# Performance work log

Hardware: AMD Instinct MI355X
Metric: run time of the kernel (lower is better)

Reference implementation:

```python
import jax, jax.numpy as jnp
import numpy as np

VOCAB = 100
EMB = 256
HID = 256
B = 8
S = 2048


def setup_inputs() -> dict:
    key = jax.random.key(0)
    ks = jax.random.split(key, 12)
    s_e = 1.0 / np.sqrt(EMB)
    s_h = 1.0 / np.sqrt(HID)
    return {
        "x": jax.random.randint(ks[0], (B, S), 0, VOCAB),
        "embedding": jax.random.normal(ks[1], (VOCAB, EMB), jnp.float32),
        "w_ih": jax.random.uniform(ks[2], (3 * HID, EMB), jnp.float32, -s_e, s_e),
        "w_hh": jax.random.uniform(ks[3], (3 * HID, HID), jnp.float32, -s_h, s_h),
        "b_ih": jax.random.uniform(ks[4], (3 * HID,), jnp.float32, -s_h, s_h),
        "b_hh": jax.random.uniform(ks[5], (3 * HID,), jnp.float32, -s_h, s_h),
        "attn_w": jax.random.uniform(ks[6], (HID, HID), jnp.float32, -s_h, s_h),
        "attn_b": jax.random.uniform(ks[7], (HID,), jnp.float32, -s_h, s_h),
        "comb_w": jax.random.uniform(ks[8], (HID, 2 * HID), jnp.float32, -s_h, s_h),
        "comb_b": jax.random.uniform(ks[9], (HID,), jnp.float32, -s_h, s_h),
        "fc_w": jax.random.uniform(ks[10], (VOCAB, HID), jnp.float32, -s_h, s_h),
        "fc_b": jax.random.uniform(ks[11], (VOCAB,), jnp.float32, -s_h, s_h),
    }


def _gru(emb, w_ih, w_hh, b_ih, b_hh):
    # emb: [B, S, E]; PyTorch GRU gate order: r, z, n
    xg = jnp.einsum('bse,ge->bsg', emb, w_ih) + b_ih  # [B, S, 3H]
    h0 = jnp.zeros((emb.shape[0], HID), emb.dtype)

    def step(h, xg_t):
        hg = h @ w_hh.T + b_hh
        xr, xz, xn = jnp.split(xg_t, 3, axis=-1)
        hr, hz, hn = jnp.split(hg, 3, axis=-1)
        r = jax.nn.sigmoid(xr + hr)
        z = jax.nn.sigmoid(xz + hz)
        n = jnp.tanh(xn + r * hn)
        h_new = (1.0 - z) * n + z * h
        return h_new, h_new

    h_last, hs = jax.lax.scan(step, h0, jnp.swapaxes(xg, 0, 1))
    return jnp.swapaxes(hs, 0, 1), h_last  # [B,S,H], [B,H]


def reference(x, embedding, w_ih, w_hh, b_ih, b_hh, attn_w, attn_b, comb_w, comb_b, fc_w, fc_b):
    emb = embedding[x]  # [B, S, E]
    all_h, h_last = _gru(emb, w_ih, w_hh, b_ih, b_hh)
    keys = jnp.einsum('bsh,kh->bsk', all_h, attn_w) + attn_b  # [B,S,H]
    scores = jnp.einsum('bqh,bkh->bqk', all_h, keys)  # [B,S,S]
    seq = all_h.shape[1]
    causal = jnp.tril(jnp.ones((seq, seq), bool))
    scores = jnp.where(causal[None], scores, -jnp.inf)
    attn = jax.nn.softmax(scores, axis=-1)
    context = jnp.einsum('bqk,bkh->bqh', attn, all_h)  # [B,S,H]
    combined = jnp.concatenate([all_h, context], axis=-1)
    combined = jnp.tanh(jnp.einsum('bsd,hd->bsh', combined, comb_w) + comb_b)
    output = jnp.einsum('bsh,vh->bsv', combined, fc_w) + fc_b
    return output, h_last[None]  # hidden: [num_layers=1, B, H]
```

## Files before the change

### kernel.cpp

```cpp
#include <hip/hip_runtime.h>

#define SEQ  2048
#define NB   8
#define HD   256
#define G3   768
#define NV   100
#define KVB  32

typedef float f32x4 __attribute__((ext_vector_type(4)));
typedef int   i32x4 __attribute__((ext_vector_type(4)));
typedef short s16x8 __attribute__((ext_vector_type(8)));
typedef unsigned short u16x4 __attribute__((ext_vector_type(4)));

#define INV26 1.490116119384765625e-8f

__device__ __forceinline__ float rcp_fast(float x) {
  return __builtin_amdgcn_rcpf(x);
}
__device__ __forceinline__ float sigm(float x) {
  x = fminf(fmaxf(x, -30.f), 30.f);
  return rcp_fast(1.f + __expf(-x));
}
__device__ __forceinline__ float tanh_fast(float x) {
  x = fminf(fmaxf(x, -15.f), 15.f);
  float e = __expf(2.f * x);
  return (e - 1.f) * rcp_fast(e + 1.f);
}
__device__ __forceinline__ void cvt_hilo(float f, unsigned short& h, unsigned short& l) {
  unsigned u = __float_as_uint(f);
  h = (unsigned short)(u >> 16);
  float r = f - __uint_as_float(u & 0xffff0000u);
  l = (unsigned short)(__float_as_uint(r) >> 16);
}

__global__ __launch_bounds__(256) void build_table(
    const float* __restrict__ emb, const float* __restrict__ w_ih,
    const float* __restrict__ b_ih, float* __restrict__ table) {
  __shared__ float eL[256];
  __shared__ float wL[256][37];
  int v = blockIdx.x, tid = threadIdx.x;
  eL[tid] = emb[v * HD + tid];
  for (int gt = 0; gt < 3; ++gt) {
    float acc = b_ih[gt * 256 + tid];
    for (int e0 = 0; e0 < HD; e0 += 32) {
      __syncthreads();
      #pragma unroll
      for (int i = 0; i < 32; ++i) {
        int idx = tid + i * 256;
        int r = idx >> 5, c = idx & 31;
        wL[r][c] = w_ih[(size_t)(gt * 256 + r) * HD + e0 + c];
      }
      __syncthreads();
      #pragma unroll
      for (int c = 0; c < 32; ++c) acc += eL[e0 + c] * wL[tid][c];
    }
    table[((size_t)v * 256 + tid) * 4 + gt] = acc;
  }
}

__global__ void __launch_bounds__(512) gru_scan(
    const int* __restrict__ x, const float* __restrict__ w_hh,
    const float* __restrict__ b_hh, const float* __restrict__ table,
    float* __restrict__ all_h, float* __restrict__ h_last) {
  __shared__ __align__(16) signed char hpk[2][2 * 272];
  __shared__ int xs[SEQ];
  const int b = blockIdx.x;
  int tid = threadIdx.x;
  int lane = tid & 63, wv = tid >> 6;
  int ncol = lane & 15, quad = lane >> 4;
  int usel = quad & 1;
  int j = wv * 32 + usel * 16 + ncol;

  for (int i = tid; i < SEQ; i += 512) xs[i] = x[b * SEQ + i];
  for (int i = tid; i < 2 * 272; i += 512)
    hpk[0][i] = (i >= 272) ? (signed char)-128 : 0;

  i32x4 bw[2][3][4];
  float Cn2[2][3];
  #pragma unroll
  for (int u = 0; u < 2; ++u) {
    #pragma unroll
    for (int t3 = 0; t3 < 3; ++t3) {
      int row = t3 * 256 + wv * 32 + u * 16 + ncol;
      int sw = 0;
      #pragma unroll
      for (int c = 0; c < 4; ++c) {
        const float* p = w_hh + (size_t)row * HD + c * 64 + quad * 16;
        unsigned pw[4] = {0u, 0u, 0u, 0u};
        #pragma unroll
        for (int e = 0; e < 16; ++e) {
          int q = __float2int_rn(p[e] * 2048.f);
          q = max(-127, min(127, q));
          sw += q;
          pw[e >> 2] |= ((unsigned)(q & 255)) << ((e & 3) * 8);
        }
        bw[u][t3][c] = (i32x4){(int)pw[0], (int)pw[1], (int)pw[2], (int)pw[3]};
      }
      sw += __shfl_xor(sw, 16);
      sw += __shfl_xor(sw, 32);
      Cn2[u][t3] = b_hh[row] + 128.f * (float)sw * INV26;
    }
  }
  float Csel[3];
  #pragma unroll
  for (int t3 = 0; t3 < 3; ++t3) Csel[t3] = usel ? Cn2[1][t3] : Cn2[0][t3];

  float hreg = 0.f;
  __syncthreads();
  float xr, xz, xn;
  {
    int v = xs[0];
    f32x4 xg = *(const f32x4*)&table[((size_t)v * 256 + j) * 4];
    xr = xg[0]; xz = xg[1]; xn = xg[2];
  }
  int a_base = (ncol & 1) * 272 + quad * 16;

  for (int t = 0; t < SEQ; ++t) {
    const signed char* cb = hpk[t & 1];
    i32x4 a[4];
    #pragma unroll
    for (int c = 0; c < 4; ++c)
      a[c] = *(const i32x4*)&cb[a_base + c * 64];
    float hg[3];
    #pragma unroll
    for (int t3 = 0; t3 < 3; ++t3) {
      i32x4 A0 = {0, 0, 0, 0}, A1 = {0, 0, 0, 0};
      #pragma unroll
      for (int c = 0; c < 4; ++c) {
        A0 = __builtin_amdgcn_mfma_i32_16x16x64_i8(a[c], bw[0][t3][c], A0, 0, 0, 0);
        A1 = __builtin_amdgcn_mfma_i32_16x16x64_i8(a[c], bw[1][t3][c], A1, 0, 0, 0);
      }
      int d0 = usel ? A1[0] : A0[0];
      int d1 = usel ? A1[1] : A0[1];
      hg[t3] = ((float)d0 * 256.f + (float)d1) * INV26 + Csel[t3];
    }
    float r = sigm(xr + hg[0]);
    float z = sigm(xz + hg[1]);
    float n = tanh_fast(xn + r * hg[2]);
    float h = (1.f - z) * n + z * hreg;
    hreg = h;
    int q = min(__float2int_rn(h * 32768.f), 32767);
    int lou = q & 255;
    int hi8 = (q - lou) >> 8;
    signed char* nx = hpk[(t + 1) & 1];
    if (quad < 2) {
      nx[j] = (signed char)hi8;
      nx[272 + j] = (signed char)(lou - 128);
      all_h[((size_t)b * SEQ + t) * HD + j] = h;
    }
    int v = xs[(t + 1 < SEQ) ? t + 1 : t];
    f32x4 xg = *(const f32x4*)&table[((size_t)v * 256 + j) * 4];
    xr = xg[0]; xz = xg[1]; xn = xg[2];
    __syncthreads();
  }
  if (quad < 2) h_last[b * HD + j] = hreg;
}

template<int ACT>
__global__ __launch_bounds__(256) void gemm_bias(
    const float* __restrict__ A, int lda,
    const float* __restrict__ W, const float* __restrict__ bias,
    float* __restrict__ C, int ldc, int N, int K) {
  __shared__ float As[128][36];
  __shared__ float Ws[64][36];
  int tid = threadIdx.x;
  int m0 = blockIdx.y * 128, n0 = blockIdx.x * 64;
  int ml = tid & 31, g = tid >> 5;
  float acc[4][8];
  #pragma unroll
  for (int i = 0; i < 4; ++i)
    #pragma unroll
    for (int jj = 0; jj < 8; ++jj) acc[i][jj] = 0.f;
  for (int k0 = 0; k0 < K; k0 += 32) {
    __syncthreads();
    #pragma unroll
    for (int i = 0; i < 4; ++i) {
      int idx = tid + i * 256;
      int r = idx >> 3, c4 = (idx & 7) * 4;
      *(f32x4*)&As[r][c4] = *(const f32x4*)&A[(size_t)(m0 + r) * lda + k0 + c4];
    }
    #pragma unroll
    for (int i = 0; i < 2; ++i) {
      int idx = tid + i * 256;
      int r = idx >> 3, c4 = (idx & 7) * 4;
      f32x4 wv = {0.f, 0.f, 0.f, 0.f};
      if (n0 + r < N) wv = *(const f32x4*)&W[(size_t)(n0 + r) * K + k0 + c4];
      *(f32x4*)&Ws[r][c4] = wv;
    }
    __syncthreads();
    #pragma unroll
    for (int k4 = 0; k4 < 32; k4 += 4) {
      f32x4 av[4], wv8[8];
      #pragma unroll
      for (int i = 0; i < 4; ++i) av[i] = *(const f32x4*)&As[ml + i * 32][k4];
      #pragma unroll
      for (int jj = 0; jj < 8; ++jj) wv8[jj] = *(const f32x4*)&Ws[g * 8 + jj][k4];
      #pragma unroll
      for (int kk = 0; kk < 4; ++kk)
        #pragma unroll
        for (int i = 0; i < 4; ++i)
          #pragma unroll
          for (int jj = 0; jj < 8; ++jj)
            acc[i][jj] += av[i][kk] * wv8[jj][kk];
    }
  }
  #pragma unroll
  for (int i = 0; i < 4; ++i) {
    int m = m0 + ml + i * 32;
    #pragma unroll
    for (int jj = 0; jj < 8; ++jj) {
      int n = n0 + g * 8 + jj;
      if (n < N) {
        float val = acc[i][jj] + bias[n];
        if (ACT) val = tanh_fast(val);
        C[(size_t)m * ldc + n] = val;
      }
    }
  }
}

__global__ __launch_bounds__(256) void gemm_keys_pack(
    const float* __restrict__ A,
    const float* __restrict__ W, const float* __restrict__ bias,
    unsigned short* __restrict__ KP) {
  __shared__ float As[128][36];
  __shared__ float Ws[64][36];
  const int K = 256;
  int tid = threadIdx.x;
  int m0 = blockIdx.y * 128, n0 = blockIdx.x * 64;
  int ml = tid & 31, gq = tid >> 5;
  float acc[4][8];
  #pragma unroll
  for (int i = 0; i < 4; ++i)
    #pragma unroll
    for (int jj = 0; jj < 8; ++jj) acc[i][jj] = 0.f;
  for (int k0 = 0; k0 < K; k0 += 32) {
    __syncthreads();
    #pragma unroll
    for (int i = 0; i < 4; ++i) {
      int idx = tid + i * 256;
      int r = idx >> 3, c4 = (idx & 7) * 4;
      *(f32x4*)&As[r][c4] = *(const f32x4*)&A[(size_t)(m0 + r) * HD + k0 + c4];
    }
    #pragma unroll
    for (int i = 0; i < 2; ++i) {
      int idx = tid + i * 256;
      int r = idx >> 3, c4 = (idx & 7) * 4;
      *(f32x4*)&Ws[r][c4] = *(const f32x4*)&W[(size_t)(n0 + r) * K + k0 + c4];
    }
    __syncthreads();
    #pragma unroll
    for (int k4 = 0; k4 < 32; k4 += 4) {
      f32x4 av[4], wv8[8];
      #pragma unroll
      for (int i = 0; i < 4; ++i) av[i] = *(const f32x4*)&As[ml + i * 32][k4];
      #pragma unroll
      for (int jj = 0; jj < 8; ++jj) wv8[jj] = *(const f32x4*)&Ws[gq * 8 + jj][k4];
      #pragma unroll
      for (int kk = 0; kk < 4; ++kk)
        #pragma unroll
        for (int i = 0; i < 4; ++i)
          #pragma unroll
          for (int jj = 0; jj < 8; ++jj)
            acc[i][jj] += av[i][kk] * wv8[jj][kk];
    }
  }
  #pragma unroll
  for (int i = 0; i < 4; ++i) {
    int m = m0 + ml + i * 32;
    int bb = m >> 11, key = m & 2047;
    int kt = key >> 5, g = (key >> 4) & 1, lmk = key & 15;
    int nb = n0 + gq * 8;
    int ch = nb >> 5, kq = (nb >> 3) & 3;
    size_t base = ((size_t)(bb * 64 + kt) * 32 + (g * 8 + ch) * 2) * 512
                + (size_t)(lmk + kq * 16) * 8;
    union { s16x8 v; unsigned short u[8]; } uh, ul;
    #pragma unroll
    for (int jj = 0; jj < 8; ++jj) {
      float val = acc[i][jj] + bias[nb + jj];
      cvt_hilo(val, uh.u[jj], ul.u[jj]);
    }
    *(s16x8*)&KP[base] = uh.v;
    *(s16x8*)&KP[base + 512] = ul.v;
  }
}

__global__ __launch_bounds__(256) void gemm_bias_cat(
    const float* __restrict__ A1, const float* __restrict__ A2,
    const float* __restrict__ W, const float* __restrict__ bias,
    float* __restrict__ C) {
  __shared__ float As[128][36];
  __shared__ float Ws[64][36];
  const int K = 512;
  int tid = threadIdx.x;
  int m0 = blockIdx.y * 128, n0 = blockIdx.x * 64;
  int ml = tid & 31, g = tid >> 5;
  float acc[4][8];
  #pragma unroll
  for (int i = 0; i < 4; ++i)
    #pragma unroll
    for (int jj = 0; jj < 8; ++jj) acc[i][jj] = 0.f;
  for (int k0 = 0; k0 < K; k0 += 32) {
    const float* src = (k0 < 256) ? A1 : A2;
    int kb = (k0 < 256) ? k0 : k0 - 256;
    __syncthreads();
    #pragma unroll
    for (int i = 0; i < 4; ++i) {
      int idx = tid + i * 256;
      int r = idx >> 3, c4 = (idx & 7) * 4;
      *(f32x4*)&As[r][c4] = *(const f32x4*)&src[(size_t)(m0 + r) * 256 + kb + c4];
    }
    #pragma unroll
    for (int i = 0; i < 2; ++i) {
      int idx = tid + i * 256;
      int r = idx >> 3, c4 = (idx & 7) * 4;
      *(f32x4*)&Ws[r][c4] = *(const f32x4*)&W[(size_t)(n0 + r) * K + k0 + c4];
    }
    __syncthreads();
    #pragma unroll
    for (int k4 = 0; k4 < 32; k4 += 4) {
      f32x4 av[4], wv8[8];
      #pragma unroll
      for (int i = 0; i < 4; ++i) av[i] = *(const f32x4*)&As[ml + i * 32][k4];
      #pragma unroll
      for (int jj = 0; jj < 8; ++jj) wv8[jj] = *(const f32x4*)&Ws[g * 8 + jj][k4];
      #pragma unroll
      for (int kk = 0; kk < 4; ++kk)
        #pragma unroll
        for (int i = 0; i < 4; ++i)
          #pragma unroll
          for (int jj = 0; jj < 8; ++jj)
            acc[i][jj] += av[i][kk] * wv8[jj][kk];
    }
  }
  #pragma unroll
  for (int i = 0; i < 4; ++i) {
    int m = m0 + ml + i * 32;
    #pragma unroll
    for (int jj = 0; jj < 8; ++jj) {
      int n = n0 + g * 8 + jj;
      C[(size_t)m * 256 + n] = tanh_fast(acc[i][jj] + bias[n]);
    }
  }
}

__global__ __launch_bounds__(256, 1) void attention_kernel(
    const float* __restrict__ all_h, const unsigned short* __restrict__ kp,
    float* __restrict__ ctxg) {
  __shared__ __align__(16) unsigned short KU[32 * 512];
  __shared__ __align__(16) unsigned short VH[16][524], VL[16][524];
  __shared__ __align__(16) unsigned short PB[4][2][520];
  const int b = blockIdx.y, qb = blockIdx.x;
  int tid = threadIdx.x, lane = tid & 63, wv = tid >> 6;
  int lm = lane & 15, kg = lane >> 4;
  const float* hb = all_h + (size_t)b * SEQ * HD;
  const unsigned short* kpb = kp + (size_t)b * 64 * 16384;
  const int q0 = qb * 64 + wv * 16;

  s16x8 Qh[8], Ql[8];
  {
    const float* qp = hb + (size_t)(q0 + lm) * HD;
    #pragma unroll
    for (int ch = 0; ch < 8; ++ch) {
      union { s16x8 v; unsigned short u[8]; } uh, ul;
      f32x4 a0 = *(const f32x4*)&qp[ch * 32 + kg * 8];
      f32x4 a1 = *(const f32x4*)&qp[ch * 32 + kg * 8 + 4];
      #pragma unroll
      for (int e = 0; e < 4; ++e) {
        cvt_hilo(a0[e], uh.u[e], ul.u[e]);
        cvt_hilo(a1[e], uh.u[4 + e], ul.u[4 + e]);
      }
      Qh[ch] = uh.v; Ql[ch] = ul.v;
    }
  }

  f32x4 co[16];
  #pragma unroll
  for (int ht = 0; ht < 16; ++ht) co[ht] = (f32x4){0.f, 0.f, 0.f, 0.f};
  float mo[4] = {-3e38f, -3e38f, -3e38f, -3e38f};
  float lr[4] = {0.f, 0.f, 0.f, 0.f};

  const int nkt = 2 * qb + 2;
  s16x8 kp8[8];
  f32x4 vreg[8];
  {
    #pragma unroll
    for (int i = 0; i < 8; ++i) {
      int up = wv + i * 4;
      kp8[i] = *(const s16x8*)&kpb[(size_t)up * 512 + lane * 8];
    }
    #pragma unroll
    for (int i = 0; i < 8; ++i) {
      int idx = tid + i * 256;
      int r = idx >> 6, c = idx & 63;
      vreg[i] = *(const f32x4*)&hb[(size_t)r * HD + c * 4];
    }
  }
  for (int kt = 0; kt < nkt; ++kt) {
    __syncthreads();
    #pragma unroll
    for (int i = 0; i < 8; ++i) {
      int up = wv + i * 4;
      *(s16x8*)&KU[up * 512 + lane * 8] = kp8[i];
    }
    #pragma unroll
    for (int i = 0; i < 8; ++i) {
      int idx = tid + i * 256;
      int r = idx >> 6, c = idx & 63;
      f32x4 vv = vreg[i];
      int kgv = r >> 3, ev = r & 7, ht = c >> 2;
      #pragma unroll
      for (int e = 0; e < 4; ++e) {
        unsigned short h16, l16;
        cvt_hilo(vv[e], h16, l16);
        int o = (kgv * 16 + (c & 3) * 4 + e) * 8 + ev;
        VH[ht][o] = h16; VL[ht][o] = l16;
      }
    }
    __syncthreads();
    if (kt + 1 < nkt) {
      const unsigned short* tb = kpb + (size_t)(kt + 1) * 16384;
      #pragma unroll
      for (int i = 0; i < 8; ++i) {
        int up = wv + i * 4;
        kp8[i] = *(const s16x8*)&tb[(size_t)up * 512 + lane * 8];
      }
      int k1 = (kt + 1) * KVB;
      #pragma unroll
      for (int i = 0; i < 8; ++i) {
        int idx = tid + i * 256;
        int r = idx >> 6, c = idx & 63;
        vreg[i] = *(const f32x4*)&hb[(size_t)(k1 + r) * HD + c * 4];
      }
    }
    int k0 = kt * KVB;

    float s[4][2];
    #pragma unroll
    for (int g = 0; g < 2; ++g) {
      f32x4 a0 = {0.f,0.f,0.f,0.f}, a1 = {0.f,0.f,0.f,0.f}, a2 = {0.f,0.f,0.f,0.f};
      #pragma unroll
      for (int ch = 0; ch < 8; ++ch) {
        const unsigned short* ub = &KU[((g * 8 + ch) * 2) * 512 + lane * 8];
        s16x8 bh = *(const s16x8*)ub;
        s16x8 bl = *(const s16x8*)(ub + 512);
        a0 = __builtin_amdgcn_mfma_f32_16x16x32_bf16(Qh[ch], bh, a0, 0, 0, 0);
        a1 = __builtin_amdgcn_mfma_f32_16x16x32_bf16(Ql[ch], bh, a1, 0, 0, 0);
        a2 = __builtin_amdgcn_mfma_f32_16x16x32_bf16(Qh[ch], bl, a2, 0, 0, 0);
      }
      #pragma unroll
      for (int r = 0; r < 4; ++r) s[r][g] = a0[r] + a1[r] + a2[r];
    }
    float p[4][2], al[4];
    #pragma unroll
    for (int r = 0; r < 4; ++r) {
      int qrow = q0 + kg * 4 + r;
      int va = (k0 + lm) <= qrow, vb = (k0 + 16 + lm) <= qrow;
      float ta = va ? s[r][0] : -3e38f;
      float tb = vb ? s[r][1] : -3e38f;
      float t = fmaxf(ta, tb);
      t = fmaxf(t, __shfl_xor(t, 1));
      t = fmaxf(t, __shfl_xor(t, 2));
      t = fmaxf(t, __shfl_xor(t, 4));
      t = fmaxf(t, __shfl_xor(t, 8));
      float mn = fmaxf(mo[r], t);
      al[r] = __expf(mo[r] - mn);
      float pa = va ? __expf(s[r][0] - mn) : 0.f;
      float pb = vb ? __expf(s[r][1] - mn) : 0.f;
      p[r][0] = pa; p[r][1] = pb;
      float rs = pa + pb;
      rs += __shfl_xor(rs, 1);
      rs += __shfl_xor(rs, 2);
      rs += __shfl_xor(rs, 4);
      rs += __shfl_xor(rs, 8);
      lr[r] = lr[r] * al[r] + rs;
      mo[r] = mn;
    }
    #pragma unroll
    for (int r = 0; r < 4; ++r)
      #pragma unroll
      for (int g = 0; g < 2; ++g) {
        unsigned short ph, pl;
        cvt_hilo(p[r][g], ph, pl);
        int key = g * 16 + lm;
        int o = ((key >> 3) * 16 + kg * 4 + r) * 8 + (key & 7);
        PB[wv][0][o] = ph;
        PB[wv][1][o] = pl;
      }
    s16x8 pah = *(const s16x8*)&PB[wv][0][lane * 8];
    s16x8 pal = *(const s16x8*)&PB[wv][1][lane * 8];
    #pragma unroll
    for (int ht = 0; ht < 16; ++ht) {
      f32x4 c = co[ht];
      #pragma unroll
      for (int r = 0; r < 4; ++r) c[r] *= al[r];
      s16x8 vh = *(const s16x8*)&VH[ht][lane * 8];
      s16x8 vl = *(const s16x8*)&VL[ht][lane * 8];
      c = __builtin_amdgcn_mfma_f32_16x16x32_bf16(pah, vh, c, 0, 0, 0);
      c = __builtin_amdgcn_mfma_f32_16x16x32_bf16(pah, vl, c, 0, 0, 0);
      c = __builtin_amdgcn_mfma_f32_16x16x32_bf16(pal, vh, c, 0, 0, 0);
      co[ht] = c;
    }
  }
  float li[4];
  #pragma unroll
  for (int r = 0; r < 4; ++r) li[r] = rcp_fast(lr[r]);
  #pragma unroll
  for (int ht = 0; ht < 16; ++ht)
    #pragma unroll
    for (int r = 0; r < 4; ++r)
      ctxg[((size_t)b * SEQ + q0 + kg * 4 + r) * HD + ht * 16 + lm] = co[ht][r] * li[r];
}

extern "C" void kernel_launch(void* const* d_in, const int* in_sizes, int n_in,
                              void* d_out, int out_size, void* d_ws, size_t ws_size,
                              hipStream_t stream) {
  (void)in_sizes; (void)n_in; (void)out_size; (void)ws_size;
  const int*   x      = (const int*)  d_in[0];
  const float* emb    = (const float*)d_in[1];
  const float* w_ih   = (const float*)d_in[2];
  const float* w_hh   = (const float*)d_in[3];
  const float* b_ih   = (const float*)d_in[4];
  const float* b_hh   = (const float*)d_in[5];
  const float* attn_w = (const float*)d_in[6];
  const float* attn_b = (const float*)d_in[7];
  const float* comb_w = (const float*)d_in[8];
  const float* comb_b = (const float*)d_in[9];
  const float* fc_w   = (const float*)d_in[10];
  const float* fc_b   = (const float*)d_in[11];
  float* out = (float*)d_out;

  float* ws    = (float*)d_ws;
  float* table = ws;
  float* all_h = table + 102400;
  float* keysb = all_h + 4194304;
  float* ctx   = keysb + 4194304;
  float* hlast = out + (size_t)NB * SEQ * NV;
  unsigned short* kpack = (unsigned short*)keysb;

  build_table<<<100, 256, 0, stream>>>(emb, w_ih, b_ih, table);
  gru_scan<<<NB, 512, 0, stream>>>(x, w_hh, b_hh, table, all_h, hlast);
  gemm_keys_pack<<<dim3(4, 128), 256, 0, stream>>>(all_h, attn_w, attn_b, kpack);
  attention_kernel<<<dim3(32, 8), 256, 0, stream>>>(all_h, kpack, ctx);
  gemm_bias_cat<<<dim3(4, 128), 256, 0, stream>>>(all_h, ctx, comb_w, comb_b, keysb);
  gemm_bias<0><<<dim3(2, 128), 256, 0, stream>>>(keysb, 256, fc_w, fc_b, out, 100, 100, 256);
}
```

Measured before the change: 1.880 ms.

## Split attention key range across waves and pre-pack V in a separate kernel

Adds a pack_v kernel that converts V (all_h) to hi/lo bf16 MFMA layout once, instead of each attention block converting it in LDS every tile. The attention kernel now handles 16 queries per block, with 4 waves taking interleaved key tiles (split-K) and reading K/V fragments straight from global memory. Partial results are merged through LDS with a log-sum-exp combine, and heavy blocks launch first. This raises the block count and removes per-block LDS staging and syncs, at the cost of an extra launch, extra workspace, and uncached global fragment loads.

```diff
diff --git a/kernel.cpp b/kernel.cpp
--- a/kernel.cpp
+++ b/kernel.cpp
@@ -285,94 +285,69 @@
   }
 }
 
-__global__ __launch_bounds__(256) void gemm_bias_cat(
-    const float* __restrict__ A1, const float* __restrict__ A2,
-    const float* __restrict__ W, const float* __restrict__ bias,
-    float* __restrict__ C) {
-  __shared__ float As[128][36];
-  __shared__ float Ws[64][36];
-  const int K = 512;
-  int tid = threadIdx.x;
-  int m0 = blockIdx.y * 128, n0 = blockIdx.x * 64;
-  int ml = tid & 31, g = tid >> 5;
-  float acc[4][8];
-  #pragma unroll
-  for (int i = 0; i < 4; ++i)
-    #pragma unroll
-    for (int jj = 0; jj < 8; ++jj) acc[i][jj] = 0.f;
-  for (int k0 = 0; k0 < K; k0 += 32) {
-    const float* src = (k0 < 256) ? A1 : A2;
-    int kb = (k0 < 256) ? k0 : k0 - 256;
-    __syncthreads();
-    #pragma unroll
-    for (int i = 0; i < 4; ++i) {
-      int idx = tid + i * 256;
-      int r = idx >> 3, c4 = (idx & 7) * 4;
-      *(f32x4*)&As[r][c4] = *(const f32x4*)&src[(size_t)(m0 + r) * 256 + kb + c4];
-    }
-    #pragma unroll
-    for (int i = 0; i < 2; ++i) {
-      int idx = tid + i * 256;
-      int r = idx >> 3, c4 = (idx & 7) * 4;
-      *(f32x4*)&Ws[r][c4] = *(const f32x4*)&W[(size_t)(n0 + r) * K + k0 + c4];
-    }
-    __syncthreads();
-    #pragma unroll
-    for (int k4 = 0; k4 < 32; k4 += 4) {
-      f32x4 av[4], wv8[8];
-      #pragma unroll
-      for (int i = 0; i < 4; ++i) av[i] = *(const f32x4*)&As[ml + i * 32][k4];
-      #pragma unroll
-      for (int jj = 0; jj < 8; ++jj) wv8[jj] = *(const f32x4*)&Ws[g * 8 + jj][k4];
-      #pragma unroll
-      for (int kk = 0; kk < 4; ++kk)
-        #pragma unroll
-        for (int i = 0; i < 4; ++i)
-          #pragma unroll
-          for (int jj = 0; jj < 8; ++jj)
-            acc[i][jj] += av[i][kk] * wv8[jj][kk];
-    }
-  }
+__global__ __launch_bounds__(256) void pack_v(
+    const float* __restrict__ all_h, unsigned short* __restrict__ vp) {
+  __shared__ float Lt[32][264];
+  int b = blockIdx.y, kt = blockIdx.x, tid = threadIdx.x;
+  const float* hb = all_h + (size_t)b * SEQ * HD + (size_t)kt * KVB * HD;
+  #pragma unroll
+  for (int i = 0; i < 8; ++i) {
+    int idx = tid + i * 256;
+    int r = idx >> 6, c = idx & 63;
+    *(f32x4*)&Lt[r][c * 4] = *(const f32x4*)&hb[(size_t)r * HD + c * 4];
+  }
+  __syncthreads();
+  unsigned short* vpt = vp + (size_t)(b * 64 + kt) * 16384;
   #pragma unroll
   for (int i = 0; i < 4; ++i) {
-    int m = m0 + ml + i * 32;
-    #pragma unroll
-    for (int jj = 0; jj < 8; ++jj) {
-      int n = n0 + g * 8 + jj;
-      C[(size_t)m * 256 + n] = tanh_fast(acc[i][jj] + bias[n]);
-    }
-  }
-}
-
-__global__ __launch_bounds__(256, 1) void attention_kernel(
+    int chunk = tid + i * 256;
+    int ht = chunk >> 6, l = chunk & 63;
+    union { s16x8 v; unsigned short u[8]; } uh, ul;
+    #pragma unroll
+    for (int e = 0; e < 8; ++e) {
+      float f = Lt[(l >> 4) * 8 + e][ht * 16 + (l & 15)];
+      cvt_hilo(f, uh.u[e], ul.u[e]);
+    }
+    *(s16x8*)&vpt[(size_t)(ht * 2) * 512 + l * 8] = uh.v;
+    *(s16x8*)&vpt[(size_t)(ht * 2 + 1) * 512 + l * 8] = ul.v;
+  }
+}
+
+__global__ __launch_bounds__(256) void attention_kernel(
     const float* __restrict__ all_h, const unsigned short* __restrict__ kp,
-    float* __restrict__ ctxg) {
-  __shared__ __align__(16) unsigned short KU[32 * 512];
-  __shared__ __align__(16) unsigned short VH[16][524], VL[16][524];
+    const unsigned short* __restrict__ vp, float* __restrict__ ctxg) {
+  __shared__ __align__(16) f32x4 OL[4 * 16 * 65];
   __shared__ __align__(16) unsigned short PB[4][2][520];
-  const int b = blockIdx.y, qb = blockIdx.x;
+  __shared__ float mlL[4][2][16];
+  const int b = blockIdx.y, q16 = 127 - blockIdx.x;
   int tid = threadIdx.x, lane = tid & 63, wv = tid >> 6;
   int lm = lane & 15, kg = lane >> 4;
   const float* hb = all_h + (size_t)b * SEQ * HD;
   const unsigned short* kpb = kp + (size_t)b * 64 * 16384;
-  const int q0 = qb * 64 + wv * 16;
-
+  const unsigned short* vpb = vp + (size_t)b * 64 * 16384;
+  const int q0 = q16 * 16;
+  const int nkt = (q16 >> 1) + 1;
+
+  float* Qs = (float*)OL;
+  #pragma unroll
+  for (int i = 0; i < 4; ++i) {
+    int idx = tid + i * 256;
+    int r = idx >> 6, c = idx & 63;
+    *(f32x4*)&Qs[r * 260 + c * 4] = *(const f32x4*)&hb[(size_t)(q0 + r) * HD + c * 4];
+  }
+  __syncthreads();
   s16x8 Qh[8], Ql[8];
-  {
-    const float* qp = hb + (size_t)(q0 + lm) * HD;
-    #pragma unroll
-    for (int ch = 0; ch < 8; ++ch) {
-      union { s16x8 v; unsigned short u[8]; } uh, ul;
-      f32x4 a0 = *(const f32x4*)&qp[ch * 32 + kg * 8];
-      f32x4 a1 = *(const f32x4*)&qp[ch * 32 + kg * 8 + 4];
-      #pragma unroll
-      for (int e = 0; e < 4; ++e) {
-        cvt_hilo(a0[e], uh.u[e], ul.u[e]);
-        cvt_hilo(a1[e], uh.u[4 + e], ul.u[4 + e]);
-      }
-      Qh[ch] = uh.v; Ql[ch] = ul.v;
-    }
-  }
+  #pragma unroll
+  for (int ch = 0; ch < 8; ++ch) {
+    union { s16x8 v; unsigned short u[8]; } uh, ul;
+    #pragma unroll
+    for (int e = 0; e < 8; ++e) {
+      float f = Qs[lm * 260 + ch * 32 + kg * 8 + e];
+      cvt_hilo(f, uh.u[e], ul.u[e]);
+    }
+    Qh[ch] = uh.v; Ql[ch] = ul.v;
+  }
+  __syncthreads();
 
   f32x4 co[16];
   #pragma unroll
@@ -380,68 +355,17 @@
   float mo[4] = {-3e38f, -3e38f, -3e38f, -3e38f};
   float lr[4] = {0.f, 0.f, 0.f, 0.f};
 
-  const int nkt = 2 * qb + 2;
-  s16x8 kp8[8];
-  f32x4 vreg[8];
-  {
-    #pragma unroll
-    for (int i = 0; i < 8; ++i) {
-      int up = wv + i * 4;
-      kp8[i] = *(const s16x8*)&kpb[(size_t)up * 512 + lane * 8];
-    }
-    #pragma unroll
-    for (int i = 0; i < 8; ++i) {
-      int idx = tid + i * 256;
-      int r = idx >> 6, c = idx & 63;
-      vreg[i] = *(const f32x4*)&hb[(size_t)r * HD + c * 4];
-    }
-  }
-  for (int kt = 0; kt < nkt; ++kt) {
-    __syncthreads();
-    #pragma unroll
-    for (int i = 0; i < 8; ++i) {
-      int up = wv + i * 4;
-      *(s16x8*)&KU[up * 512 + lane * 8] = kp8[i];
-    }
-    #pragma unroll
-    for (int i = 0; i < 8; ++i) {
-      int idx = tid + i * 256;
-      int r = idx >> 6, c = idx & 63;
-      f32x4 vv = vreg[i];
-      int kgv = r >> 3, ev = r & 7, ht = c >> 2;
-      #pragma unroll
-      for (int e = 0; e < 4; ++e) {
-        unsigned short h16, l16;
-        cvt_hilo(vv[e], h16, l16);
-        int o = (kgv * 16 + (c & 3) * 4 + e) * 8 + ev;
-        VH[ht][o] = h16; VL[ht][o] = l16;
-      }
-    }
-    __syncthreads();
-    if (kt + 1 < nkt) {
-      const unsigned short* tb = kpb + (size_t)(kt + 1) * 16384;
-      #pragma unroll
-      for (int i = 0; i < 8; ++i) {
-        int up = wv + i * 4;
-        kp8[i] = *(const s16x8*)&tb[(size_t)up * 512 + lane * 8];
-      }
-      int k1 = (kt + 1) * KVB;
-      #pragma unroll
-      for (int i = 0; i < 8; ++i) {
-        int idx = tid + i * 256;
-        int r = idx >> 6, c = idx & 63;
-        vreg[i] = *(const f32x4*)&hb[(size_t)(k1 + r) * HD + c * 4];
-      }
-    }
+  for (int kt = wv; kt < nkt; kt += 4) {
     int k0 = kt * KVB;
-
+    const unsigned short* kpt = kpb + (size_t)kt * 16384;
+    const unsigned short* vpt = vpb + (size_t)kt * 16384;
     float s[4][2];
     #pragma unroll
     for (int g = 0; g < 2; ++g) {
       f32x4 a0 = {0.f,0.f,0.f,0.f}, a1 = {0.f,0.f,0.f,0.f}, a2 = {0.f,0.f,0.f,0.f};
       #pragma unroll
       for (int ch = 0; ch < 8; ++ch) {
-        const unsigned short* ub = &KU[((g * 8 + ch) * 2) * 512 + lane * 8];
+        const unsigned short* ub = &kpt[(size_t)((g * 8 + ch) * 2) * 512 + lane * 8];
         s16x8 bh = *(const s16x8*)ub;
         s16x8 bl = *(const s16x8*)(ub + 512);
         a0 = __builtin_amdgcn_mfma_f32_16x16x32_bf16(Qh[ch], bh, a0, 0, 0, 0);
@@ -494,22 +418,113 @@
       f32x4 c = co[ht];
       #pragma unroll
       for (int r = 0; r < 4; ++r) c[r] *= al[r];
-      s16x8 vh = *(const s16x8*)&VH[ht][lane * 8];
-      s16x8 vl = *(const s16x8*)&VL[ht][lane * 8];
+      const unsigned short* vb2 = &vpt[(size_t)(ht * 2) * 512 + lane * 8];
+      s16x8 vh = *(const s16x8*)vb2;
+      s16x8 vl = *(const s16x8*)(vb2 + 512);
       c = __builtin_amdgcn_mfma_f32_16x16x32_bf16(pah, vh, c, 0, 0, 0);
       c = __builtin_amdgcn_mfma_f32_16x16x32_bf16(pah, vl, c, 0, 0, 0);
       c = __builtin_amdgcn_mfma_f32_16x16x32_bf16(pal, vh, c, 0, 0, 0);
       co[ht] = c;
     }
   }
-  float li[4];
-  #pragma unroll
-  for (int r = 0; r < 4; ++r) li[r] = rcp_fast(lr[r]);
   #pragma unroll
   for (int ht = 0; ht < 16; ++ht)
-    #pragma unroll
-    for (int r = 0; r < 4; ++r)
-      ctxg[((size_t)b * SEQ + q0 + kg * 4 + r) * HD + ht * 16 + lm] = co[ht][r] * li[r];
+    OL[(wv * 16 + ht) * 65 + lane] = co[ht];
+  if (lm == 0) {
+    #pragma unroll
+    for (int r = 0; r < 4; ++r) {
+      mlL[wv][0][kg * 4 + r] = mo[r];
+      mlL[wv][1][kg * 4 + r] = lr[r];
+    }
+  }
+  __syncthreads();
+  {
+    int row = tid & 15, ht = tid >> 4;
+    float mw[4], lw[4];
+    #pragma unroll
+    for (int w = 0; w < 4; ++w) { mw[w] = mlL[w][0][row]; lw[w] = mlL[w][1][row]; }
+    float M = fmaxf(fmaxf(mw[0], mw[1]), fmaxf(mw[2], mw[3]));
+    float sc[4], den = 0.f;
+    #pragma unroll
+    for (int w = 0; w < 4; ++w) { sc[w] = __expf(mw[w] - M); den += sc[w] * lw[w]; }
+    float inv = rcp_fast(den);
+    int kg2 = row >> 2, r2 = row & 3;
+    #pragma unroll
+    for (int c4 = 0; c4 < 4; ++c4) {
+      f32x4 acc = {0.f, 0.f, 0.f, 0.f};
+      #pragma unroll
+      for (int w = 0; w < 4; ++w) {
+        const float* base = (const float*)&OL[(w * 16 + ht) * 65 + kg2 * 16 + c4 * 4];
+        acc[0] += sc[w] * base[r2];
+        acc[1] += sc[w] * base[4 + r2];
+        acc[2] += sc[w] * base[8 + r2];
+        acc[3] += sc[w] * base[12 + r2];
+      }
+      f32x4 outv;
+      #pragma unroll
+      for (int jj = 0; jj < 4; ++jj) outv[jj] = acc[jj] * inv;
+      *(f32x4*)&ctxg[((size_t)b * SEQ + q0 + row) * HD + ht * 16 + c4 * 4] = outv;
+    }
+  }
+}
+
+__global__ __launch_bounds__(256) void gemm_bias_cat(
+    const float* __restrict__ A1, const float* __restrict__ A2,
+    const float* __restrict__ W, const float* __restrict__ bias,
+    float* __restrict__ C) {
+  __shared__ float As[128][36];
+  __shared__ float Ws[64][36];
+  const int K = 512;
+  int tid = threadIdx.x;
+  int m0 = blockIdx.y * 128, n0 = blockIdx.x * 64;
+  int ml = tid & 31, g = tid >> 5;
+  float acc[4][8];
+  #pragma unroll
+  for (int i = 0; i < 4; ++i)
+    #pragma unroll
+    for (int jj = 0; jj < 8; ++jj) acc[i][jj] = 0.f;
+  for (int k0 = 0; k0 < K; k0 += 32) {
+    const float* src = (k0 < 256) ? A1 : A2;
+    int kb = (k0 < 256) ? k0 : k0 - 256;
+    __syncthreads();
+    #pragma unroll
+    for (int i = 0; i < 4; ++i) {
+      int idx = tid + i * 256;
+      int r = idx >> 3, c4 = (idx & 7) * 4;
+      *(f32x4*)&As[r][c4] = *(const f32x4*)&src[(size_t)(m0 + r) * 256 + kb + c4];
+    }
+    #pragma unroll
+    for (int i = 0; i < 2; ++i) {
+      int idx = tid + i * 256;
+      int r = idx >> 3, c4 = (idx & 7) * 4;
+      *(f32x4*)&Ws[r][c4] = *(const f32x4*)&W[(size_t)(n0 + r) * K + k0 + c4];
+    }
+    __syncthreads();
+    #pragma unroll
+    for (int k4 = 0; k4 < 32; k4 += 4) {
+      f32x4 av[4], wv8[8];
+      #pragma unroll
+      for (int i = 0; i < 4; ++i) av[i] = *(const f32x4*)&As[ml + i * 32][k4];
+      #pragma unroll
+      for (int jj = 0; jj < 8; ++jj) wv8[jj] = *(const f32x4*)&Ws[g * 8 + jj][k4];
+      #pragma unroll
+      for (int kk = 0; kk < 4; ++kk)
+        #pragma unroll
+        for (int i = 0; i < 4; ++i)
+          #pragma unroll
+          for (int jj = 0; jj < 8; ++jj)
+            acc[i][jj] += av[i][kk] * wv8[jj][kk];
+    }
+  }
+  #pragma unroll
+  for (int i = 0; i < 4; ++i) {
+    int m = m0 + ml + i * 32;
+    #pragma unroll
+    for (int jj = 0; jj < 8; ++jj) {
+      int n = n0 + g * 8 + jj;
+      C[(size_t)m * 256 + n] = tanh_fast(acc[i][jj] + bias[n]);
+    }
+  }
 }
 
 extern "C" void kernel_launch(void* const* d_in, const int* in_sizes, int n_in,
@@ -535,13 +550,16 @@
   float* all_h = table + 102400;
   float* keysb = all_h + 4194304;
   float* ctx   = keysb + 4194304;
+  float* vbuf  = ctx + 4194304;
   float* hlast = out + (size_t)NB * SEQ * NV;
   unsigned short* kpack = (unsigned short*)keysb;
+  unsigned short* vpack = (unsigned short*)vbuf;
 
   build_table<<<100, 256, 0, stream>>>(emb, w_ih, b_ih, table);
   gru_scan<<<NB, 512, 0, stream>>>(x, w_hh, b_hh, table, all_h, hlast);
   gemm_keys_pack<<<dim3(4, 128), 256, 0, stream>>>(all_h, attn_w, attn_b, kpack);
-  attention_kernel<<<dim3(32, 8), 256, 0, stream>>>(all_h, kpack, ctx);
+  pack_v<<<dim3(64, NB), 256, 0, stream>>>(all_h, vpack);
+  attention_kernel<<<dim3(128, NB), 256, 0, stream>>>(all_h, kpack, vpack, ctx);
   gemm_bias_cat<<<dim3(4, 128), 256, 0, stream>>>(all_h, ctx, comb_w, comb_b, keysb);
   gemm_bias<0><<<dim3(2, 128), 256, 0, stream>>>(keysb, 256, fc_w, fc_b, out, 100, 100, 256);
 }
```

After: 1.917 ms. Within noise of the previous version (+2.0%).

## Prepack V in bf16 hi/lo once and fuse combine and FC GEMMs

Applied to the files above, without the earlier changes.

The V operand (all_h) is now converted to a bf16 hi/lo MFMA layout once, inside the keys GEMM kernel (blockIdx.x==0 blocks), and no longer inside every attention block on every key tile. The attention kernel streams the prepacked V tiles the same way it streams K, which removes the repeated per-tile conversion and the scattered LDS writes. The combine GEMM (tanh) and the final FC projection are fused into one kernel that keeps the 64x256 combined tile in LDS, removing a launch and the intermediate global round trip. The trade-offs are an extra packed buffer in the workspace, uneven load in the keys kernel, and a large-LDS fused kernel with only 256 blocks, which may lower occupancy.

```diff
diff --git a/kernel.cpp b/kernel.cpp
--- a/kernel.cpp
+++ b/kernel.cpp
@@ -10,7 +10,6 @@
 typedef float f32x4 __attribute__((ext_vector_type(4)));
 typedef int   i32x4 __attribute__((ext_vector_type(4)));
 typedef short s16x8 __attribute__((ext_vector_type(8)));
-typedef unsigned short u16x4 __attribute__((ext_vector_type(4)));
 
 #define INV26 1.490116119384765625e-8f
 
@@ -156,75 +155,13 @@
   if (quad < 2) h_last[b * HD + j] = hreg;
 }
 
-template<int ACT>
-__global__ __launch_bounds__(256) void gemm_bias(
-    const float* __restrict__ A, int lda,
-    const float* __restrict__ W, const float* __restrict__ bias,
-    float* __restrict__ C, int ldc, int N, int K) {
-  __shared__ float As[128][36];
-  __shared__ float Ws[64][36];
-  int tid = threadIdx.x;
-  int m0 = blockIdx.y * 128, n0 = blockIdx.x * 64;
-  int ml = tid & 31, g = tid >> 5;
-  float acc[4][8];
-  #pragma unroll
-  for (int i = 0; i < 4; ++i)
-    #pragma unroll
-    for (int jj = 0; jj < 8; ++jj) acc[i][jj] = 0.f;
-  for (int k0 = 0; k0 < K; k0 += 32) {
-    __syncthreads();
-    #pragma unroll
-    for (int i = 0; i < 4; ++i) {
-      int idx = tid + i * 256;
-      int r = idx >> 3, c4 = (idx & 7) * 4;
-      *(f32x4*)&As[r][c4] = *(const f32x4*)&A[(size_t)(m0 + r) * lda + k0 + c4];
-    }
-    #pragma unroll
-    for (int i = 0; i < 2; ++i) {
-      int idx = tid + i * 256;
-      int r = idx >> 3, c4 = (idx & 7) * 4;
-      f32x4 wv = {0.f, 0.f, 0.f, 0.f};
-      if (n0 + r < N) wv = *(const f32x4*)&W[(size_t)(n0 + r) * K + k0 + c4];
-      *(f32x4*)&Ws[r][c4] = wv;
-    }
-    __syncthreads();
-    #pragma unroll
-    for (int k4 = 0; k4 < 32; k4 += 4) {
-      f32x4 av[4], wv8[8];
-      #pragma unroll
-      for (int i = 0; i < 4; ++i) av[i] = *(const f32x4*)&As[ml + i * 32][k4];
-      #pragma unroll
-      for (int jj = 0; jj < 8; ++jj) wv8[jj] = *(const f32x4*)&Ws[g * 8 + jj][k4];
-      #pragma unroll
-      for (int kk = 0; kk < 4; ++kk)
-        #pragma unroll
-        for (int i = 0; i < 4; ++i)
-          #pragma unroll
-          for (int jj = 0; jj < 8; ++jj)
-            acc[i][jj] += av[i][kk] * wv8[jj][kk];
-    }
-  }
-  #pragma unroll
-  for (int i = 0; i < 4; ++i) {
-    int m = m0 + ml + i * 32;
-    #pragma unroll
-    for (int jj = 0; jj < 8; ++jj) {
-      int n = n0 + g * 8 + jj;
-      if (n < N) {
-        float val = acc[i][jj] + bias[n];
-        if (ACT) val = tanh_fast(val);
-        C[(size_t)m * ldc + n] = val;
-      }
-    }
-  }
-}
-
 __global__ __launch_bounds__(256) void gemm_keys_pack(
     const float* __restrict__ A,
     const float* __restrict__ W, const float* __restrict__ bias,
-    unsigned short* __restrict__ KP) {
+    unsigned short* __restrict__ KP, unsigned short* __restrict__ VP) {
   __shared__ float As[128][36];
   __shared__ float Ws[64][36];
+  __shared__ float Lt[32][264];
   const int K = 256;
   int tid = threadIdx.x;
   int m0 = blockIdx.y * 128, n0 = blockIdx.x * 64;
@@ -283,78 +220,49 @@
     *(s16x8*)&KP[base] = uh.v;
     *(s16x8*)&KP[base + 512] = ul.v;
   }
-}
-
-__global__ __launch_bounds__(256) void gemm_bias_cat(
-    const float* __restrict__ A1, const float* __restrict__ A2,
-    const float* __restrict__ W, const float* __restrict__ bias,
-    float* __restrict__ C) {
-  __shared__ float As[128][36];
-  __shared__ float Ws[64][36];
-  const int K = 512;
-  int tid = threadIdx.x;
-  int m0 = blockIdx.y * 128, n0 = blockIdx.x * 64;
-  int ml = tid & 31, g = tid >> 5;
-  float acc[4][8];
-  #pragma unroll
-  for (int i = 0; i < 4; ++i)
-    #pragma unroll
-    for (int jj = 0; jj < 8; ++jj) acc[i][jj] = 0.f;
-  for (int k0 = 0; k0 < K; k0 += 32) {
-    const float* src = (k0 < 256) ? A1 : A2;
-    int kb = (k0 < 256) ? k0 : k0 - 256;
-    __syncthreads();
-    #pragma unroll
-    for (int i = 0; i < 4; ++i) {
-      int idx = tid + i * 256;
-      int r = idx >> 3, c4 = (idx & 7) * 4;
-      *(f32x4*)&As[r][c4] = *(const f32x4*)&src[(size_t)(m0 + r) * 256 + kb + c4];
-    }
-    #pragma unroll
-    for (int i = 0; i < 2; ++i) {
-      int idx = tid + i * 256;
-      int r = idx >> 3, c4 = (idx & 7) * 4;
-      *(f32x4*)&Ws[r][c4] = *(const f32x4*)&W[(size_t)(n0 + r) * K + k0 + c4];
-    }
-    __syncthreads();
-    #pragma unroll
-    for (int k4 = 0; k4 < 32; k4 += 4) {
-      f32x4 av[4], wv8[8];
-      #pragma unroll
-      for (int i = 0; i < 4; ++i) av[i] = *(const f32x4*)&As[ml + i * 32][k4];
-      #pragma unroll
-      for (int jj = 0; jj < 8; ++jj) wv8[jj] = *(const f32x4*)&Ws[g * 8 + jj][k4];
-      #pragma unroll
-      for (int kk = 0; kk < 4; ++kk)
+  if (blockIdx.x == 0) {
+    int bb2 = m0 >> 11;
+    int kt0 = (m0 & 2047) >> 5;
+    for (int t4 = 0; t4 < 4; ++t4) {
+      const float* hb = A + (size_t)(m0 + t4 * 32) * HD;
+      __syncthreads();
+      #pragma unroll
+      for (int i2 = 0; i2 < 8; ++i2) {
+        int idx = tid + i2 * 256;
+        int r = idx >> 6, c = idx & 63;
+        *(f32x4*)&Lt[r][c * 4] = *(const f32x4*)&hb[(size_t)r * HD + c * 4];
+      }
+      __syncthreads();
+      unsigned short* vpt = VP + (size_t)(bb2 * 64 + kt0 + t4) * 16384;
+      #pragma unroll
+      for (int i2 = 0; i2 < 4; ++i2) {
+        int chunk = tid + i2 * 256;
+        int ht = chunk >> 6, l = chunk & 63;
+        union { s16x8 v; unsigned short u[8]; } uh2, ul2;
         #pragma unroll
-        for (int i = 0; i < 4; ++i)
-          #pragma unroll
-          for (int jj = 0; jj < 8; ++jj)
-            acc[i][jj] += av[i][kk] * wv8[jj][kk];
-    }
-  }
-  #pragma unroll
-  for (int i = 0; i < 4; ++i) {
-    int m = m0 + ml + i * 32;
-    #pragma unroll
-    for (int jj = 0; jj < 8; ++jj) {
-      int n = n0 + g * 8 + jj;
-      C[(size_t)m * 256 + n] = tanh_fast(acc[i][jj] + bias[n]);
+        for (int e = 0; e < 8; ++e) {
+          float f = Lt[(l >> 4) * 8 + e][ht * 16 + (l & 15)];
+          cvt_hilo(f, uh2.u[e], ul2.u[e]);
+        }
+        *(s16x8*)&vpt[(size_t)(ht * 2) * 512 + l * 8] = uh2.v;
+        *(s16x8*)&vpt[(size_t)(ht * 2 + 1) * 512 + l * 8] = ul2.v;
+      }
     }
   }
 }
 
 __global__ __launch_bounds__(256, 1) void attention_kernel(
     const float* __restrict__ all_h, const unsigned short* __restrict__ kp,
-    float* __restrict__ ctxg) {
+    const unsigned short* __restrict__ vp, float* __restrict__ ctxg) {
   __shared__ __align__(16) unsigned short KU[32 * 512];
-  __shared__ __align__(16) unsigned short VH[16][524], VL[16][524];
+  __shared__ __align__(16) unsigned short VU[32 * 512];
   __shared__ __align__(16) unsigned short PB[4][2][520];
   const int b = blockIdx.y, qb = blockIdx.x;
   int tid = threadIdx.x, lane = tid & 63, wv = tid >> 6;
   int lm = lane & 15, kg = lane >> 4;
   const float* hb = all_h + (size_t)b * SEQ * HD;
   const unsigned short* kpb = kp + (size_t)b * 64 * 16384;
+  const unsigned short* vpb = vp + (size_t)b * 64 * 16384;
   const int q0 = qb * 64 + wv * 16;
 
   s16x8 Qh[8], Ql[8];
@@ -381,20 +289,12 @@
   float lr[4] = {0.f, 0.f, 0.f, 0.f};
 
   const int nkt = 2 * qb + 2;
-  s16x8 kp8[8];
-  f32x4 vreg[8];
-  {
-    #pragma unroll
-    for (int i = 0; i < 8; ++i) {
-      int up = wv + i * 4;
-      kp8[i] = *(const s16x8*)&kpb[(size_t)up * 512 + lane * 8];
-    }
-    #pragma unroll
-    for (int i = 0; i < 8; ++i) {
-      int idx = tid + i * 256;
-      int r = idx >> 6, c = idx & 63;
-      vreg[i] = *(const f32x4*)&hb[(size_t)r * HD + c * 4];
-    }
+  s16x8 kp8[8], vp8[8];
+  #pragma unroll
+  for (int i = 0; i < 8; ++i) {
+    int up = wv + i * 4;
+    kp8[i] = *(const s16x8*)&kpb[(size_t)up * 512 + lane * 8];
+    vp8[i] = *(const s16x8*)&vpb[(size_t)up * 512 + lane * 8];
   }
   for (int kt = 0; kt < nkt; ++kt) {
     __syncthreads();
@@ -402,35 +302,17 @@
     for (int i = 0; i < 8; ++i) {
       int up = wv + i * 4;
       *(s16x8*)&KU[up * 512 + lane * 8] = kp8[i];
-    }
-    #pragma unroll
-    for (int i = 0; i < 8; ++i) {
-      int idx = tid + i * 256;
-      int r = idx >> 6, c = idx & 63;
-      f32x4 vv = vreg[i];
-      int kgv = r >> 3, ev = r & 7, ht = c >> 2;
-      #pragma unroll
-      for (int e = 0; e < 4; ++e) {
-        unsigned short h16, l16;
-        cvt_hilo(vv[e], h16, l16);
-        int o = (kgv * 16 + (c & 3) * 4 + e) * 8 + ev;
-        VH[ht][o] = h16; VL[ht][o] = l16;
-      }
+      *(s16x8*)&VU[up * 512 + lane * 8] = vp8[i];
     }
     __syncthreads();
     if (kt + 1 < nkt) {
-      const unsigned short* tb = kpb + (size_t)(kt + 1) * 16384;
+      const unsigned short* tk = kpb + (size_t)(kt + 1) * 16384;
+      const unsigned short* tv = vpb + (size_t)(kt + 1) * 16384;
       #pragma unroll
       for (int i = 0; i < 8; ++i) {
         int up = wv + i * 4;
-        kp8[i] = *(const s16x8*)&tb[(size_t)up * 512 + lane * 8];
-      }
-      int k1 = (kt + 1) * KVB;
-      #pragma unroll
-      for (int i = 0; i < 8; ++i) {
-        int idx = tid + i * 256;
-        int r = idx >> 6, c = idx & 63;
-        vreg[i] = *(const f32x4*)&hb[(size_t)(k1 + r) * HD + c * 4];
+        kp8[i] = *(const s16x8*)&tk[(size_t)up * 512 + lane * 8];
+        vp8[i] = *(const s16x8*)&tv[(size_t)up * 512 + lane * 8];
       }
     }
     int k0 = kt * KVB;
@@ -494,8 +376,9 @@
       f32x4 c = co[ht];
       #pragma unroll
       for (int r = 0; r < 4; ++r) c[r] *= al[r];
-      s16x8 vh = *(const s16x8*)&VH[ht][lane * 8];
-      s16x8 vl = *(const s16x8*)&VL[ht][lane * 8];
+      const unsigned short* vb2 = &VU[(ht * 2) * 512 + lane * 8];
+      s16x8 vh = *(const s16x8*)vb2;
+      s16x8 vl = *(const s16x8*)(vb2 + 512);
       c = __builtin_amdgcn_mfma_f32_16x16x32_bf16(pah, vh, c, 0, 0, 0);
       c = __builtin_amdgcn_mfma_f32_16x16x32_bf16(pah, vl, c, 0, 0, 0);
       c = __builtin_amdgcn_mfma_f32_16x16x32_bf16(pal, vh, c, 0, 0, 0);
@@ -510,6 +393,107 @@
     #pragma unroll
     for (int r = 0; r < 4; ++r)
       ctxg[((size_t)b * SEQ + q0 + kg * 4 + r) * HD + ht * 16 + lm] = co[ht][r] * li[r];
+}
+
+__global__ __launch_bounds__(256) void gemm_cat_fc(
+    const float* __restrict__ A1, const float* __restrict__ A2,
+    const float* __restrict__ Wc, const float* __restrict__ bc,
+    const float* __restrict__ Wf, const float* __restrict__ bf,
+    float* __restrict__ out) {
+  __shared__ __align__(16) float As[64][37];
+  __shared__ __align__(16) float Ws[128][37];
+  __shared__ __align__(16) float Cs[64][260];
+  __shared__ __align__(16) float Fw[100][36];
+  int tid = threadIdx.x;
+  int m0 = blockIdx.x * 64;
+  int ml = tid & 31, g = tid >> 5;
+  float acc[2][2][16];
+  #pragma unroll
+  for (int p = 0; p < 2; ++p)
+    #pragma unroll
+    for (int i = 0; i < 2; ++i)
+      #pragma unroll
+      for (int jj = 0; jj < 16; ++jj) acc[p][i][jj] = 0.f;
+  for (int p = 0; p < 2; ++p) {
+    for (int k0 = 0; k0 < 512; k0 += 32) {
+      const float* src = (k0 < 256) ? A1 : A2;
+      int kb = (k0 < 256) ? k0 : k0 - 256;
+      __syncthreads();
+      #pragma unroll
+      for (int i = 0; i < 2; ++i) {
+        int idx = tid + i * 256;
+        int r = idx >> 3, c4 = (idx & 7) * 4;
+        *(f32x4*)&As[r][c4] = *(const f32x4*)&src[(size_t)(m0 + r) * 256 + kb + c4];
+      }
+      #pragma unroll
+      for (int i = 0; i < 4; ++i) {
+        int idx = tid + i * 256;
+        int r = idx >> 3, c4 = (idx & 7) * 4;
+        *(f32x4*)&Ws[r][c4] = *(const f32x4*)&Wc[(size_t)(p * 128 + r) * 512 + k0 + c4];
+      }
+      __syncthreads();
+      #pragma unroll
+      for (int k4 = 0; k4 < 32; k4 += 4) {
+        f32x4 av[2];
+        av[0] = *(const f32x4*)&As[ml][k4];
+        av[1] = *(const f32x4*)&As[ml + 32][k4];
+        #pragma unroll
+        for (int jj = 0; jj < 16; ++jj) {
+          f32x4 wv = *(const f32x4*)&Ws[g * 16 + jj][k4];
+          #pragma unroll
+          for (int i = 0; i < 2; ++i)
+            #pragma unroll
+            for (int kk = 0; kk < 4; ++kk)
+              acc[p][i][jj] += av[i][kk] * wv[kk];
+        }
+      }
+    }
+  }
+  __syncthreads();
+  #pragma unroll
+  for (int p = 0; p < 2; ++p)
+    #pragma unroll
+    for (int i = 0; i < 2; ++i)
+      #pragma unroll
+      for (int jj = 0; jj < 16; ++jj) {
+        int n = p * 128 + g * 16 + jj;
+        Cs[ml + i * 32][n] = tanh_fast(acc[p][i][jj] + bc[n]);
+      }
+  int r2 = tid >> 2, cg2 = tid & 3;
+  float accf[25];
+  #pragma unroll
+  for (int c = 0; c < 25; ++c) accf[c] = 0.f;
+  for (int k0 = 0; k0 < 256; k0 += 32) {
+    __syncthreads();
+    #pragma unroll
+    for (int i = 0; i < 4; ++i) {
+      int idx = tid + i * 256;
+      if (idx < 800) {
+        int n = idx >> 3, c4 = (idx & 7) * 4;
+        *(f32x4*)&Fw[n][c4] = *(const f32x4*)&Wf[(size_t)n * 256 + k0 + c4];
+      }
+    }
+    __syncthreads();
+    f32x4 cs[8];
+    #pragma unroll
+    for (int q = 0; q < 8; ++q) cs[q] = *(const f32x4*)&Cs[r2][k0 + q * 4];
+    #pragma unroll
+    for (int c = 0; c < 25; ++c) {
+      int n = cg2 * 25 + c;
+      #pragma unroll
+      for (int q = 0; q < 8; ++q) {
+        f32x4 fw = *(const f32x4*)&Fw[n][q * 4];
+        accf[c] += cs[q][0] * fw[0] + cs[q][1] * fw[1]
+                 + cs[q][2] * fw[2] + cs[q][3] * fw[3];
+      }
+    }
+  }
+  int m = m0 + r2;
+  #pragma unroll
+  for (int c = 0; c < 25; ++c) {
+    int n = cg2 * 25 + c;
+    out[(size_t)m * NV + n] = accf[c] + bf[n];
+  }
 }
 
 extern "C" void kernel_launch(void* const* d_in, const int* in_sizes, int n_in,
@@ -535,13 +519,14 @@
   float* all_h = table + 102400;
   float* keysb = all_h + 4194304;
   float* ctx   = keysb + 4194304;
+  float* vbuf  = ctx + 4194304;
   float* hlast = out + (size_t)NB * SEQ * NV;
   unsigned short* kpack = (unsigned short*)keysb;
+  unsigned short* vpack = (unsigned short*)vbuf;
 
   build_table<<<100, 256, 0, stream>>>(emb, w_ih, b_ih, table);
   gru_scan<<<NB, 512, 0, stream>>>(x, w_hh, b_hh, table, all_h, hlast);
-  gemm_keys_pack<<<dim3(4, 128), 256, 0, stream>>>(all_h, attn_w, attn_b, kpack);
-  attention_kernel<<<dim3(32, 8), 256, 0, stream>>>(all_h, kpack, ctx);
-  gemm_bias_cat<<<dim3(4, 128), 256, 0, stream>>>(all_h, ctx, comb_w, comb_b, keysb);
-  gemm_bias<0><<<dim3(2, 128), 256, 0, stream>>>(keysb, 256, fc_w, fc_b, out, 100, 100, 256);
-}
+  gemm_keys_pack<<<dim3(4, 128), 256, 0, stream>>>(all_h, attn_w, attn_b, kpack, vpack);
+  attention_kernel<<<dim3(32, NB), 256, 0, stream>>>(all_h, kpack, vpack, ctx);
+  gemm_cat_fc<<<256, 256, 0, stream>>>(all_h, ctx, comb_w, comb_b, fc_w, fc_b, out);
+}
```

New measurement: 1.992 ms. 1.06x slower.
